# Performance work log

Hardware: AMD Instinct MI355X
Metric: run time of the kernel (lower is better)

Reference implementation:

```python
import jax, jax.numpy as jnp
import numpy as np

N, E, B = 30000, 240000, 64
F, H, T = 64, 4, 3
BOT = 256


def _gat_layer(x, e_src, e_dst, lin_w, att_src, att_dst, bias):
    # x: [N, in]; lin_w: [in, H*F]; att_*: [H, F]; bias: [H*F]
    xs = (x @ lin_w).reshape(N, H, F)                     # [N,H,F]
    a_src = jnp.einsum('nhf,hf->nh', xs, att_src)         # [N,H]
    a_dst = jnp.einsum('nhf,hf->nh', xs, att_dst)
    logits = jax.nn.leaky_relu(a_src[e_src] + a_dst[e_dst], negative_slope=0.2)  # [E2,H]
    m = jax.ops.segment_max(logits, e_dst, num_segments=N)        # softmax over in-edges per dst
    ex = jnp.exp(logits - m[e_dst])
    denom = jax.ops.segment_sum(ex, e_dst, num_segments=N)
    alpha = ex / (denom[e_dst] + 1e-16)                   # [E2,H]
    msg = alpha[:, :, None] * xs[e_src]                   # [E2,H,F]
    out = jax.ops.segment_sum(msg, e_dst, num_segments=N).reshape(N, H * F)
    return out + bias


def setup_inputs() -> dict:
    key = jax.random.key(0)
    ks = jax.random.split(key, 20)
    s = 0.1
    inp = {
        'street_feature': jax.random.normal(ks[0], (N, 5), jnp.float32),
        'edge_index': jax.random.randint(ks[1], (2, E), 0, N, dtype=jnp.int64),
        'batch': jnp.sort(jax.random.randint(ks[2], (N,), 0, B, dtype=jnp.int64)),
        'bbox_w': jax.random.normal(ks[3], (5, F), jnp.float32) * s,
        'bbox_b': jnp.zeros((F,), jnp.float32),
        'lin_w0': jax.random.normal(ks[4], (F, H * F), jnp.float32) * s,
        'att_src0': jax.random.normal(ks[5], (H, F), jnp.float32) * s,
        'att_dst0': jax.random.normal(ks[6], (H, F), jnp.float32) * s,
        'bias0': jnp.zeros((H * F,), jnp.float32),
        'lin_w1': jax.random.normal(ks[7], (H * F, H * F), jnp.float32) * s,
        'att_src1': jax.random.normal(ks[8], (H, F), jnp.float32) * s,
        'att_dst1': jax.random.normal(ks[9], (H, F), jnp.float32) * s,
        'bias1': jnp.zeros((H * F,), jnp.float32),
        'lin_w2': jax.random.normal(ks[10], (H * F, H * F), jnp.float32) * s,
        'att_src2': jax.random.normal(ks[11], (H, F), jnp.float32) * s,
        'att_dst2': jax.random.normal(ks[12], (H, F), jnp.float32) * s,
        'bias2': jnp.zeros((H * F,), jnp.float32),
        'agg_w': jax.random.normal(ks[13], (F * (1 + H * T), BOT), jnp.float32) * s,
        'agg_b': jnp.zeros((BOT,), jnp.float32),
    }
    return inp


def reference(street_feature, edge_index, batch,
              bbox_w, bbox_b,
              lin_w0, att_src0, att_dst0, bias0,
              lin_w1, att_src1, att_dst1, bias1,
              lin_w2, att_src2, att_dst2, bias2,
              agg_w, agg_b):
    # add self-loops (PyG GATConv default add_self_loops=True)
    loop = jnp.arange(N, dtype=edge_index.dtype)
    e_src = jnp.concatenate([edge_index[0], loop])
    e_dst = jnp.concatenate([edge_index[1], loop])

    x = jax.nn.relu(street_feature @ bbox_w + bbox_b)            # [N,F]
    g = [jax.ops.segment_max(x, batch, num_segments=B)]          # global max pool

    layers = [(lin_w0, att_src0, att_dst0, bias0),
              (lin_w1, att_src1, att_dst1, bias1),
              (lin_w2, att_src2, att_dst2, bias2)]
    for lw, asrc, adst, b in layers:
        x = jax.nn.relu(_gat_layer(x, e_src, e_dst, lw, asrc, adst, b))  # [N,H*F]
        g.append(jax.ops.segment_max(x, batch, num_segments=B))

    g_embed = jnp.concatenate(g, axis=1)                          # [B, F*(1+H*T)]
    return g_embed @ agg_w + agg_b                                # [B, BOT]
```

## Files before the change

### kernel.cpp

```cpp
#include <hip/hip_runtime.h>
#include <hip/hip_bf16.h>

#define N_NODES 30000
#define N_EDGES 240000
#define NB      64
#define FDIM    64
#define NH      4
#define HF      256
#define E2      (N_EDGES + N_NODES)
#define GCOLS   832
#define BOTD    256
#define DEGCAP  64
#define PSPLIT  16
#define FSPLIT  8

typedef __hip_bfloat16 bf16;
typedef __attribute__((ext_vector_type(8))) short short8;
typedef __attribute__((ext_vector_type(4))) float f32x4;

#define LDA 40

__device__ __forceinline__ float b2f(bf16 v) { return __bfloat162float(v); }

#define ENC_B   7500
#define ADJ_B   1055
#define BOFF_B  118
#define WT0 (HF * FDIM)
#define WT1 (WT0 + HF * HF)
#define WT2 (WT1 + HF * HF)
#define WCONV_B 576
#define GZ_B    208
#define OZ_B    64
#define PRO_B   (ENC_B + ADJ_B + BOFF_B + WCONV_B + GZ_B + OZ_B)

__global__ __launch_bounds__(256) void prologue_kernel(
        const float* __restrict__ sf, const float* __restrict__ bw,
        const float* __restrict__ bb, bf16* __restrict__ xenc,
        const int* __restrict__ esrc, const int* __restrict__ edst,
        int* __restrict__ deg, unsigned short* __restrict__ adj,
        const int* __restrict__ batch, int* __restrict__ boff,
        const float* __restrict__ w0, const float* __restrict__ w1,
        const float* __restrict__ w2, bf16* __restrict__ wT,
        float* __restrict__ g, float* __restrict__ dout) {
    int b = blockIdx.x, t = threadIdx.x;
    if (b < ENC_B) {
        int i = b * 256 + t;
        int n = i >> 6, f = i & 63;
        float acc = bb[f];
#pragma unroll
        for (int k = 0; k < 5; ++k)
            acc += sf[n * 5 + k] * bw[k * FDIM + f];
        xenc[i] = __float2bfloat16(fmaxf(acc, 0.f));
    } else if (b < ENC_B + ADJ_B) {
        int e = (b - ENC_B) * 256 + t;
        if (e >= E2) return;
        int s, d;
        if (e < N_EDGES) { s = esrc[e]; d = edst[e]; }
        else             { s = d = e - N_EDGES; }
        int pos = atomicAdd(&deg[d], 1);
        if (pos < DEGCAP) adj[d * DEGCAP + pos] = (unsigned short)s;
    } else if (b < ENC_B + ADJ_B + BOFF_B) {
        int n = (b - ENC_B - ADJ_B) * 256 + t;
        if (n >= N_NODES) return;
        int b1 = batch[n];
        int b0 = (n == 0) ? -1 : batch[n - 1];
        for (int x = b0 + 1; x <= b1; ++x) boff[x] = n;
        if (n == N_NODES - 1)
            for (int x = b1 + 1; x <= NB; ++x) boff[x] = N_NODES;
    } else if (b < ENC_B + ADJ_B + BOFF_B + WCONV_B) {
        int i = (b - ENC_B - ADJ_B - BOFF_B) * 256 + t;
        if (i < WT0) {
            int n = i / FDIM, k = i - n * FDIM;
            wT[i] = __float2bfloat16(w0[k * HF + n]);
        } else if (i < WT1) {
            int j = i - WT0, n = j >> 8, k = j & 255;
            wT[i] = __float2bfloat16(w1[k * HF + n]);
        } else if (i < WT2) {
            int j = i - WT1, n = j >> 8, k = j & 255;
            wT[i] = __float2bfloat16(w2[k * HF + n]);
        }
    } else if (b < ENC_B + ADJ_B + BOFF_B + WCONV_B + GZ_B) {
        g[(b - ENC_B - ADJ_B - BOFF_B - WCONV_B) * 256 + t] = 0.f;
    } else {
        dout[(b - ENC_B - ADJ_B - BOFF_B - WCONV_B - GZ_B) * 256 + t] = 0.f;
    }
}

template <int K>
__global__ __launch_bounds__(256) void gemm_mfma_kernel(
        const bf16* __restrict__ xb, const bf16* __restrict__ wT,
        bf16* __restrict__ y, const float* __restrict__ asrc,
        const float* __restrict__ adst, float* __restrict__ a_s,
        float* __restrict__ a_d) {
    __shared__ short sA[64 * LDA];
    __shared__ short sB[256 * LDA];
    int t = threadIdx.x, w = t >> 6, l = t & 63;
    int q = l >> 4, m = l & 15;
    int n0 = blockIdx.x * 64;
    const short* xg = (const short*)xb;
    const short* wg = (const short*)wT;
    int ar = t >> 2, ac = t & 3;
    f32x4 acc[4][4];
#pragma unroll
    for (int rt = 0; rt < 4; ++rt)
#pragma unroll
        for (int ct = 0; ct < 4; ++ct)
            acc[rt][ct] = (f32x4){0.f, 0.f, 0.f, 0.f};

    short8 pa = {0, 0, 0, 0, 0, 0, 0, 0};
    short8 pb[4];
    if (n0 + ar < N_NODES) pa = *(const short8*)&xg[(long)(n0 + ar) * K + ac * 8];
#pragma unroll
    for (int u = 0; u < 4; ++u)
        pb[u] = *(const short8*)&wg[(long)t * K + u * 8];

#pragma unroll
    for (int k0 = 0; k0 < K; k0 += 32) {
        *(short8*)&sA[ar * LDA + ac * 8] = pa;
        {
            short* dst = &sB[t * LDA];
#pragma unroll
            for (int u = 0; u < 4; ++u) *(short8*)&dst[u * 8] = pb[u];
        }
        __syncthreads();
        if (k0 + 32 < K) {
            pa = (short8){0, 0, 0, 0, 0, 0, 0, 0};
            if (n0 + ar < N_NODES)
                pa = *(const short8*)&xg[(long)(n0 + ar) * K + k0 + 32 + ac * 8];
#pragma unroll
            for (int u = 0; u < 4; ++u)
                pb[u] = *(const short8*)&wg[(long)t * K + k0 + 32 + u * 8];
        }
        short8 af[4], bfr[4];
#pragma unroll
        for (int rt = 0; rt < 4; ++rt)
            af[rt] = *(const short8*)&sA[(16 * rt + m) * LDA + q * 8];
#pragma unroll
        for (int ct = 0; ct < 4; ++ct)
            bfr[ct] = *(const short8*)&sB[(64 * w + 16 * ct + m) * LDA + q * 8];
#pragma unroll
        for (int rt = 0; rt < 4; ++rt)
#pragma unroll
            for (int ct = 0; ct < 4; ++ct)
                acc[rt][ct] = __builtin_amdgcn_mfma_f32_16x16x32_bf16(
                    af[rt], bfr[ct], acc[rt][ct], 0, 0, 0);
        __syncthreads();
    }

#pragma unroll
    for (int rt = 0; rt < 4; ++rt)
#pragma unroll
        for (int reg = 0; reg < 4; ++reg) {
            int row = n0 + 16 * rt + 4 * q + reg;
            if (row < N_NODES) {
#pragma unroll
                for (int ct = 0; ct < 4; ++ct)
                    y[(long)row * HF + 64 * w + 16 * ct + m] =
                        __float2bfloat16(acc[rt][ct][reg]);
            }
        }
    float vs[4], vd[4];
#pragma unroll
    for (int ct = 0; ct < 4; ++ct) {
        vs[ct] = asrc[64 * w + 16 * ct + m];
        vd[ct] = adst[64 * w + 16 * ct + m];
    }
#pragma unroll
    for (int rt = 0; rt < 4; ++rt)
#pragma unroll
        for (int reg = 0; reg < 4; ++reg) {
            float ps = 0.f, pd = 0.f;
#pragma unroll
            for (int ct = 0; ct < 4; ++ct) {
                ps += acc[rt][ct][reg] * vs[ct];
                pd += acc[rt][ct][reg] * vd[ct];
            }
#pragma unroll
            for (int mask = 1; mask <= 8; mask <<= 1) {
                ps += __shfl_xor(ps, mask, 64);
                pd += __shfl_xor(pd, mask, 64);
            }
            if (m == 0) {
                int row = n0 + 16 * rt + 4 * q + reg;
                if (row < N_NODES) {
                    a_s[row * NH + w] = ps;
                    a_d[row * NH + w] = pd;
                }
            }
        }
}

__global__ __launch_bounds__(256) void agg_kernel(
        const unsigned short* __restrict__ adj, const int* __restrict__ deg,
        const bf16* __restrict__ xs, const float* __restrict__ a_s,
        const float* __restrict__ a_d, const float* __restrict__ bias,
        bf16* __restrict__ xout) {
    int n = blockIdx.x;
    int t = threadIdx.x;
    int h = t >> 6, j = t & 63;
    __shared__ unsigned short s_src[DEGCAP];
    __shared__ float s_ex[NH * DEGCAP];
    __shared__ float s_rden[NH];
    int dn = min(deg[n], DEGCAP);
    if (t < DEGCAP) s_src[t] = (t < dn) ? adj[n * DEGCAP + t] : (unsigned short)0;
    __syncthreads();
    float adh = a_d[n * NH + h];
    float ex = 0.f;
    if (j < dn) {
        int src = s_src[j];
        float a = a_s[src * NH + h] + adh;
        a = (a > 0.f) ? a : 0.2f * a;
        ex = __expf(a);
    }
    s_ex[t] = ex;
    float sum = ex;
#pragma unroll
    for (int off = 32; off > 0; off >>= 1) sum += __shfl_down(sum, off, 64);
    if (j == 0) s_rden[h] = 1.f / (sum + 1e-16f);
    __syncthreads();
    s_ex[t] *= s_rden[t >> 6];
    __syncthreads();
    float acc = 0.f;
    int dn8 = (dn + 7) & ~7;
    for (int k = 0; k < dn8; k += 8) {
        int s0 = s_src[k],     s1 = s_src[k + 1], s2 = s_src[k + 2], s3 = s_src[k + 3];
        int s4 = s_src[k + 4], s5 = s_src[k + 5], s6 = s_src[k + 6], s7 = s_src[k + 7];
        float a0 = s_ex[h * DEGCAP + k];
        float a1 = s_ex[h * DEGCAP + k + 1];
        float a2 = s_ex[h * DEGCAP + k + 2];
        float a3 = s_ex[h * DEGCAP + k + 3];
        float a4 = s_ex[h * DEGCAP + k + 4];
        float a5 = s_ex[h * DEGCAP + k + 5];
        float a6 = s_ex[h * DEGCAP + k + 6];
        float a7 = s_ex[h * DEGCAP + k + 7];
        float v0 = b2f(xs[(long)s0 * HF + t]);
        float v1 = b2f(xs[(long)s1 * HF + t]);
        float v2 = b2f(xs[(long)s2 * HF + t]);
        float v3 = b2f(xs[(long)s3 * HF + t]);
        float v4 = b2f(xs[(long)s4 * HF + t]);
        float v5 = b2f(xs[(long)s5 * HF + t]);
        float v6 = b2f(xs[(long)s6 * HF + t]);
        float v7 = b2f(xs[(long)s7 * HF + t]);
        acc += a0 * v0; acc += a1 * v1; acc += a2 * v2; acc += a3 * v3;
        acc += a4 * v4; acc += a5 * v5; acc += a6 * v6; acc += a7 * v7;
    }
    xout[(long)n * HF + t] = __float2bfloat16(fmaxf(acc + bias[t], 0.f));
}

__global__ __launch_bounds__(256) void pool256_kernel(const bf16* __restrict__ x,
                                                      const int* __restrict__ boff,
                                                      unsigned int* __restrict__ g, int goff) {
    int b = blockIdx.x / PSPLIT, part = blockIdx.x % PSPLIT;
    int t = threadIdx.x;
    int s = boff[b], e = boff[b + 1];
    int chunk = (e - s + PSPLIT - 1) / PSPLIT;
    int cs = s + part * chunk, ce = min(cs + chunk, e);
    if (cs >= ce) return;
    float v0 = 0.f, v1 = 0.f;
    int n = cs;
    for (; n + 1 < ce; n += 2) {
        v0 = fmaxf(v0, b2f(x[(long)n * HF + t]));
        v1 = fmaxf(v1, b2f(x[(long)(n + 1) * HF + t]));
    }
    if (n < ce) v0 = fmaxf(v0, b2f(x[(long)n * HF + t]));
    atomicMax(&g[b * GCOLS + goff + t], __float_as_uint(fmaxf(v0, v1)));
}

__global__ __launch_bounds__(256) void pool64_kernel(const bf16* __restrict__ x,
                                                     const int* __restrict__ boff,
                                                     unsigned int* __restrict__ g) {
    int b = blockIdx.x / PSPLIT, part = blockIdx.x % PSPLIT;
    int t = threadIdx.x, c = t & 63, r = t >> 6;
    int s = boff[b], e = boff[b + 1];
    int chunk = (e - s + PSPLIT - 1) / PSPLIT;
    int cs = s + part * chunk, ce = min(cs + chunk, e);
    __shared__ float sm[256];
    float v = 0.f;
    for (int n = cs + r; n < ce; n += 4)
        v = fmaxf(v, b2f(x[(long)n * FDIM + c]));
    sm[t] = v;
    __syncthreads();
    if (t < 64 && cs < ce) {
        float m = fmaxf(fmaxf(sm[t], sm[t + 64]), fmaxf(sm[t + 128], sm[t + 192]));
        atomicMax(&g[b * GCOLS + t], __float_as_uint(m));
    }
}

__global__ __launch_bounds__(256) void final_kernel(
        const float* __restrict__ g, const float* __restrict__ w,
        const float* __restrict__ b, float* __restrict__ outp) {
    int bb = blockIdx.x & (NB - 1);
    int slice = blockIdx.x >> 6;
    int j = threadIdx.x;
    const int KS = GCOLS / FSPLIT;
    float acc = (slice == 0) ? b[j] : 0.f;
    int k0 = slice * KS;
    for (int k = k0; k < k0 + KS; ++k)
        acc += g[bb * GCOLS + k] * w[k * BOTD + j];
    atomicAdd(&outp[bb * BOTD + j], acc);
}

extern "C" void kernel_launch(void* const* d_in, const int* in_sizes, int n_in,
                              void* d_out, int out_size, void* d_ws, size_t ws_size,
                              hipStream_t stream) {
    const float* sf     = (const float*)d_in[0];
    const int*   eidx   = (const int*)d_in[1];
    const int*   batch  = (const int*)d_in[2];
    const float* bbox_w = (const float*)d_in[3];
    const float* bbox_b = (const float*)d_in[4];
    const float* lin_w[3] = {(const float*)d_in[5],  (const float*)d_in[9],  (const float*)d_in[13]};
    const float* att_s[3] = {(const float*)d_in[6],  (const float*)d_in[10], (const float*)d_in[14]};
    const float* att_d[3] = {(const float*)d_in[7],  (const float*)d_in[11], (const float*)d_in[15]};
    const float* bias[3]  = {(const float*)d_in[8],  (const float*)d_in[12], (const float*)d_in[16]};
    const float* agg_w  = (const float*)d_in[17];
    const float* agg_b  = (const float*)d_in[18];

    const int* esrc = eidx;
    const int* edst = eidx + N_EDGES;

    char* ws = (char*)d_ws;
    bf16* xsb  = (bf16*)ws;  ws += (size_t)N_NODES * HF * 2;
    bf16* xb0  = (bf16*)ws;  ws += (size_t)N_NODES * HF * 2;
    bf16* xb1  = (bf16*)ws;  ws += (size_t)N_NODES * HF * 2;
    bf16* xenc = (bf16*)ws;  ws += (size_t)N_NODES * FDIM * 2;
    float* a_s = (float*)ws; ws += (size_t)N_NODES * NH * 4;
    float* a_d = (float*)ws; ws += (size_t)N_NODES * NH * 4;
    float* g   = (float*)ws; ws += (size_t)NB * GCOLS * 4;
    int*   deg = (int*)ws;   ws += (size_t)N_NODES * 4;
    int*   boff= (int*)ws;   ws += (size_t)(NB + 1) * 4;
    unsigned short* adj = (unsigned short*)ws; ws += (size_t)N_NODES * DEGCAP * 2;
    bf16* wT   = (bf16*)ws;  ws += (size_t)WT2 * 2;

    hipMemsetAsync(deg, 0, (size_t)N_NODES * 4, stream);
    prologue_kernel<<<PRO_B, 256, 0, stream>>>(
        sf, bbox_w, bbox_b, xenc, esrc, edst, deg, adj, batch, boff,
        lin_w[0], lin_w[1], lin_w[2], wT, g, (float*)d_out);
    pool64_kernel<<<NB * PSPLIT, 256, 0, stream>>>(xenc, boff, (unsigned int*)g);

    const bf16* wTl[3] = {wT, wT + WT0, wT + WT1};
    const bf16* xin = xenc;
    bf16* xout = xb0;
    for (int l = 0; l < 3; ++l) {
        if (l == 0)
            gemm_mfma_kernel<FDIM><<<(N_NODES + 63) / 64, 256, 0, stream>>>(
                xin, wTl[l], xsb, att_s[l], att_d[l], a_s, a_d);
        else
            gemm_mfma_kernel<HF><<<(N_NODES + 63) / 64, 256, 0, stream>>>(
                xin, wTl[l], xsb, att_s[l], att_d[l], a_s, a_d);
        agg_kernel<<<N_NODES, 256, 0, stream>>>(adj, deg, xsb, a_s, a_d, bias[l], xout);
        pool256_kernel<<<NB * PSPLIT, 256, 0, stream>>>(xout, boff, (unsigned int*)g, FDIM + l * HF);
        xin = xout;
        xout = (xout == xb0) ? xb1 : xb0;
    }
    final_kernel<<<NB * FSPLIT, 256, 0, stream>>>(g, agg_w, agg_b, (float*)d_out);
}
```

Before: 336.6 us.

## Aggregate one destination node per wavefront with vectorized bf16 gathers

The GAT aggregation kernel now gives each destination node to one 64-lane wavefront instead of a full 256-thread block. Each lane computes all four heads' edge logits from a single float4 load, the softmax reduction uses wave shuffles, and block-level __syncthreads is replaced by a wave barrier. Each lane gathers four bf16 features per edge with 8-byte vector loads. The pooling kernel also switches to vectorized 4-element loads with a shared-memory reduction across waves. This cuts block count, barrier overhead and per-thread load instructions, at the cost of fewer memory requests in flight per node.

```diff
diff --git a/kernel.cpp b/kernel.cpp
--- a/kernel.cpp
+++ b/kernel.cpp
@@ -17,10 +17,14 @@
 typedef __hip_bfloat16 bf16;
 typedef __attribute__((ext_vector_type(8))) short short8;
 typedef __attribute__((ext_vector_type(4))) float f32x4;
+typedef __attribute__((ext_vector_type(4))) unsigned short u16x4;
 
 #define LDA 40
 
 __device__ __forceinline__ float b2f(bf16 v) { return __bfloat162float(v); }
+__device__ __forceinline__ float bits2f(unsigned short u) {
+    return __uint_as_float(((unsigned int)u) << 16);
+}
 
 #define ENC_B   7500
 #define ADJ_B   1055
@@ -190,80 +194,100 @@
         }
 }
 
+#define EXP_S (DEGCAP + 4)
 __global__ __launch_bounds__(256) void agg_kernel(
         const unsigned short* __restrict__ adj, const int* __restrict__ deg,
         const bf16* __restrict__ xs, const float* __restrict__ a_s,
         const float* __restrict__ a_d, const float* __restrict__ bias,
         bf16* __restrict__ xout) {
-    int n = blockIdx.x;
-    int t = threadIdx.x;
-    int h = t >> 6, j = t & 63;
-    __shared__ unsigned short s_src[DEGCAP];
-    __shared__ float s_ex[NH * DEGCAP];
-    __shared__ float s_rden[NH];
+    int w = threadIdx.x >> 6, l = threadIdx.x & 63;
+    int n = blockIdx.x * 4 + w;
+    __shared__ unsigned short s_src_all[4][DEGCAP];
+    __shared__ float s_ex_all[4][NH][EXP_S];
+    unsigned short* s_src = s_src_all[w];
+    float (*s_ex)[EXP_S] = s_ex_all[w];
     int dn = min(deg[n], DEGCAP);
-    if (t < DEGCAP) s_src[t] = (t < dn) ? adj[n * DEGCAP + t] : (unsigned short)0;
-    __syncthreads();
-    float adh = a_d[n * NH + h];
-    float ex = 0.f;
-    if (j < dn) {
-        int src = s_src[j];
-        float a = a_s[src * NH + h] + adh;
-        a = (a > 0.f) ? a : 0.2f * a;
-        ex = __expf(a);
-    }
-    s_ex[t] = ex;
-    float sum = ex;
-#pragma unroll
-    for (int off = 32; off > 0; off >>= 1) sum += __shfl_down(sum, off, 64);
-    if (j == 0) s_rden[h] = 1.f / (sum + 1e-16f);
-    __syncthreads();
-    s_ex[t] *= s_rden[t >> 6];
-    __syncthreads();
-    float acc = 0.f;
-    int dn8 = (dn + 7) & ~7;
-    for (int k = 0; k < dn8; k += 8) {
-        int s0 = s_src[k],     s1 = s_src[k + 1], s2 = s_src[k + 2], s3 = s_src[k + 3];
-        int s4 = s_src[k + 4], s5 = s_src[k + 5], s6 = s_src[k + 6], s7 = s_src[k + 7];
-        float a0 = s_ex[h * DEGCAP + k];
-        float a1 = s_ex[h * DEGCAP + k + 1];
-        float a2 = s_ex[h * DEGCAP + k + 2];
-        float a3 = s_ex[h * DEGCAP + k + 3];
-        float a4 = s_ex[h * DEGCAP + k + 4];
-        float a5 = s_ex[h * DEGCAP + k + 5];
-        float a6 = s_ex[h * DEGCAP + k + 6];
-        float a7 = s_ex[h * DEGCAP + k + 7];
-        float v0 = b2f(xs[(long)s0 * HF + t]);
-        float v1 = b2f(xs[(long)s1 * HF + t]);
-        float v2 = b2f(xs[(long)s2 * HF + t]);
-        float v3 = b2f(xs[(long)s3 * HF + t]);
-        float v4 = b2f(xs[(long)s4 * HF + t]);
-        float v5 = b2f(xs[(long)s5 * HF + t]);
-        float v6 = b2f(xs[(long)s6 * HF + t]);
-        float v7 = b2f(xs[(long)s7 * HF + t]);
-        acc += a0 * v0; acc += a1 * v1; acc += a2 * v2; acc += a3 * v3;
-        acc += a4 * v4; acc += a5 * v5; acc += a6 * v6; acc += a7 * v7;
-    }
-    xout[(long)n * HF + t] = __float2bfloat16(fmaxf(acc + bias[t], 0.f));
+    int src_l = 0;
+    if (l < dn) {
+        src_l = adj[n * DEGCAP + l];
+        s_src[l] = (unsigned short)src_l;
+    }
+    f32x4 ad4 = *(const f32x4*)&a_d[n * NH];
+    float ex[NH];
+    if (l < dn) {
+        f32x4 as4 = *(const f32x4*)&a_s[src_l * NH];
+#pragma unroll
+        for (int h = 0; h < NH; ++h) {
+            float a = as4[h] + ad4[h];
+            a = (a > 0.f) ? a : 0.2f * a;
+            ex[h] = __expf(a);
+        }
+    } else {
+#pragma unroll
+        for (int h = 0; h < NH; ++h) ex[h] = 0.f;
+    }
+#pragma unroll
+    for (int h = 0; h < NH; ++h) {
+        float s = ex[h];
+#pragma unroll
+        for (int off = 32; off > 0; off >>= 1) s += __shfl_xor(s, off, 64);
+        s_ex[h][l] = ex[h] * (1.f / (s + 1e-16f));
+    }
+    __builtin_amdgcn_wave_barrier();
+    int hh = l >> 4;
+    const unsigned short* xg = (const unsigned short*)xs;
+    f32x4 acc = {0.f, 0.f, 0.f, 0.f};
+    int k = 0;
+    for (; k + 1 < dn; k += 2) {
+        int s0 = s_src[k], s1 = s_src[k + 1];
+        float a0 = s_ex[hh][k], a1 = s_ex[hh][k + 1];
+        u16x4 v0 = *(const u16x4*)&xg[(long)s0 * HF + 4 * l];
+        u16x4 v1 = *(const u16x4*)&xg[(long)s1 * HF + 4 * l];
+#pragma unroll
+        for (int j = 0; j < 4; ++j) {
+            acc[j] += a0 * bits2f(v0[j]);
+            acc[j] += a1 * bits2f(v1[j]);
+        }
+    }
+    if (k < dn) {
+        int s0 = s_src[k];
+        float a0 = s_ex[hh][k];
+        u16x4 v0 = *(const u16x4*)&xg[(long)s0 * HF + 4 * l];
+#pragma unroll
+        for (int j = 0; j < 4; ++j) acc[j] += a0 * bits2f(v0[j]);
+    }
+    f32x4 b4 = *(const f32x4*)&bias[4 * l];
+    u16x4 o;
+#pragma unroll
+    for (int j = 0; j < 4; ++j) {
+        bf16 ob = __float2bfloat16(fmaxf(acc[j] + b4[j], 0.f));
+        o[j] = *reinterpret_cast<unsigned short*>(&ob);
+    }
+    *(u16x4*)((unsigned short*)xout + (long)n * HF + 4 * l) = o;
 }
 
 __global__ __launch_bounds__(256) void pool256_kernel(const bf16* __restrict__ x,
                                                       const int* __restrict__ boff,
                                                       unsigned int* __restrict__ g, int goff) {
     int b = blockIdx.x / PSPLIT, part = blockIdx.x % PSPLIT;
-    int t = threadIdx.x;
+    int t = threadIdx.x, w = t >> 6, l = t & 63;
     int s = boff[b], e = boff[b + 1];
     int chunk = (e - s + PSPLIT - 1) / PSPLIT;
     int cs = s + part * chunk, ce = min(cs + chunk, e);
     if (cs >= ce) return;
-    float v0 = 0.f, v1 = 0.f;
-    int n = cs;
-    for (; n + 1 < ce; n += 2) {
-        v0 = fmaxf(v0, b2f(x[(long)n * HF + t]));
-        v1 = fmaxf(v1, b2f(x[(long)(n + 1) * HF + t]));
-    }
-    if (n < ce) v0 = fmaxf(v0, b2f(x[(long)n * HF + t]));
-    atomicMax(&g[b * GCOLS + goff + t], __float_as_uint(fmaxf(v0, v1)));
+    __shared__ f32x4 sm[256];
+    const unsigned short* xg = (const unsigned short*)x;
+    f32x4 v = {0.f, 0.f, 0.f, 0.f};
+    for (int n = cs + w; n < ce; n += 4) {
+        u16x4 u = *(const u16x4*)&xg[(long)n * HF + 4 * l];
+#pragma unroll
+        for (int j = 0; j < 4; ++j) v[j] = fmaxf(v[j], bits2f(u[j]));
+    }
+    sm[t] = v;
+    __syncthreads();
+    const float* smf = (const float*)sm;
+    float m = fmaxf(fmaxf(smf[t], smf[256 + t]), fmaxf(smf[512 + t], smf[768 + t]));
+    atomicMax(&g[b * GCOLS + goff + t], __float_as_uint(m));
 }
 
 __global__ __launch_bounds__(256) void pool64_kernel(const bf16* __restrict__ x,
@@ -347,7 +371,7 @@
         else
             gemm_mfma_kernel<HF><<<(N_NODES + 63) / 64, 256, 0, stream>>>(
                 xin, wTl[l], xsb, att_s[l], att_d[l], a_s, a_d);
-        agg_kernel<<<N_NODES, 256, 0, stream>>>(adj, deg, xsb, a_s, a_d, bias[l], xout);
+        agg_kernel<<<N_NODES / 4, 256, 0, stream>>>(adj, deg, xsb, a_s, a_d, bias[l], xout);
         pool256_kernel<<<NB * PSPLIT, 256, 0, stream>>>(xout, boff, (unsigned int*)g, FDIM + l * HF);
         xin = xout;
         xout = (xout == xb0) ? xb1 : xb0;
```

Result: faster. 283.2 us (-15.9%).
